# Optimization experiments

Hardware: AMD Instinct MI355X
Metric: run time of the kernel (lower is better)

The kernel has to match this reference:

```python
import jax, jax.numpy as jnp
import numpy as np

N_NODES = 50000
N_EDGES = 1600000
N_GRAPHS = 512
IN_DIM = 64
HID = 128
OUT_DIM = 10


def setup_inputs() -> dict:
    key = jax.random.key(0)
    ks = jax.random.split(key, 12)
    x = jax.random.normal(ks[0], (N_NODES, IN_DIM), dtype=jnp.float32)
    edge_index = jax.random.randint(ks[1], (2, N_EDGES), 0, N_NODES, dtype=jnp.int64)
    batch = jnp.sort(jax.random.randint(ks[2], (N_NODES,), 0, N_GRAPHS, dtype=jnp.int64))
    edge_attr = jax.random.uniform(ks[3], (N_EDGES,), dtype=jnp.float32)
    # glorot-ish init for weights
    def lin(k, fan_in, fan_out):
        s = (6.0 / (fan_in + fan_out)) ** 0.5
        return jax.random.uniform(k, (fan_in, fan_out), minval=-s, maxval=s, dtype=jnp.float32)
    return {
        "x": x, "edge_index": edge_index, "batch": batch, "edge_attr": edge_attr,
        "W1": lin(ks[4], IN_DIM, HID), "b1": jnp.zeros((HID,), jnp.float32),
        "W2": lin(ks[5], HID, HID), "b2": jnp.zeros((HID,), jnp.float32),
        "Wm1": lin(ks[6], HID, HID), "bm1": jnp.zeros((HID,), jnp.float32),
        "Wm2": lin(ks[7], HID, OUT_DIM), "bm2": jnp.zeros((OUT_DIM,), jnp.float32),
    }


def _gcn_conv(x, edge_index, edge_weight, W, b, num_nodes):
    """PyG GCNConv: add self-loops, symmetric norm with edge weights, x@W, scatter-add, +bias."""
    loop = jnp.arange(num_nodes, dtype=edge_index.dtype)
    src = jnp.concatenate([edge_index[0], loop])
    dst = jnp.concatenate([edge_index[1], loop])
    ew = jnp.concatenate([edge_weight, jnp.ones((num_nodes,), edge_weight.dtype)])
    deg = jax.ops.segment_sum(ew, dst, num_segments=num_nodes)  # [N]
    dinv = jnp.where(deg > 0, jax.lax.rsqrt(jnp.where(deg > 0, deg, 1.0)), 0.0)
    norm = dinv[src] * ew * dinv[dst]  # [E+N]
    h = x @ W  # [N, F_out]
    msg = h[src] * norm[:, None]  # gather + scale
    out = jax.ops.segment_sum(msg, dst, num_segments=num_nodes)
    return out + b


def reference(x, edge_index, batch, edge_attr, W1, b1, W2, b2, Wm1, bm1, Wm2, bm2):
    n = x.shape[0]
    h = _gcn_conv(x, edge_index, edge_attr, W1, b1, n)
    h = jax.nn.relu(h)  # dropout = identity in eval mode
    h = _gcn_conv(h, edge_index, edge_attr, W2, b2, n)
    h = jax.nn.relu(h)
    pooled = jax.ops.segment_sum(h, batch, num_segments=N_GRAPHS)  # global_add_pool
    z = jax.nn.relu(pooled @ Wm1 + bm1)
    return z @ Wm2 + bm2  # [num_graphs, out_dim]
```

## Files before the change

### kernel.cpp

```cpp
#include <hip/hip_runtime.h>
#include <hip/hip_bf16.h>
#include <hip/hip_fp16.h>
#include <cstdint>

#define HIDC 128
#define FIXSCALE 4194304.0f
#define FIXINV   (1.0f / 4194304.0f)
#define MAXDEG 80

#define BKT_SHIFT 7
#define BKT_NODES 128
#define BKT_CAP   6144
#define BIN_TILE  8192
#define BIN_THREADS 512

typedef _Float16 half8 __attribute__((ext_vector_type(8)));
typedef float float4v __attribute__((ext_vector_type(4)));

__global__ __launch_bounds__(BIN_THREADS) void bin_kernel(
        const int* __restrict__ ei, const float* __restrict__ ea,
        unsigned long long* __restrict__ buck, unsigned int* __restrict__ tails,
        int E, int nbkt) {
    __shared__ unsigned long long rec[BIN_TILE];
    __shared__ unsigned int cnt[BIN_THREADS];
    __shared__ unsigned int startx[BIN_THREADS];
    __shared__ unsigned int cur[BIN_THREADS];
    __shared__ unsigned int gbase[BIN_THREADS];
    int t = threadIdx.x;
    int base = blockIdx.x * BIN_TILE;
    int total = E - base; if (total > BIN_TILE) total = BIN_TILE;

    cnt[t] = 0;
    __syncthreads();

    unsigned int lo[16], dv[16];
#pragma unroll
    for (int j = 0; j < 16; ++j) {
        int e = base + j * BIN_THREADS + t;
        if (e < E) {
            int s = ei[e]; int d = ei[E + e]; float w = ea[e];
            lo[j] = (unsigned int)s |
                    ((unsigned int)__half_as_ushort(__float2half_rn(w)) << 16);
            dv[j] = (unsigned int)d;
            atomicAdd(&cnt[dv[j] >> BKT_SHIFT], 1u);
        } else dv[j] = 0xffffffffu;
    }
    __syncthreads();

    startx[t] = cnt[t];
    __syncthreads();
    for (int off = 1; off < BIN_THREADS; off <<= 1) {
        unsigned int add = (t >= off) ? startx[t - off] : 0u;
        __syncthreads();
        startx[t] += add;
        __syncthreads();
    }
    unsigned int excl = startx[t] - cnt[t];
    startx[t] = excl;
    cur[t] = excl;
    if (t < nbkt) gbase[t] = atomicAdd(&tails[t], cnt[t]);
    __syncthreads();

#pragma unroll
    for (int j = 0; j < 16; ++j) {
        if (dv[j] != 0xffffffffu) {
            unsigned int p = atomicAdd(&cur[dv[j] >> BKT_SHIFT], 1u);
            rec[p] = ((unsigned long long)dv[j] << 32) | (unsigned long long)lo[j];
        }
    }
    __syncthreads();

    for (int i = t; i < total; i += BIN_THREADS) {
        unsigned long long r = rec[i];
        unsigned int b = ((unsigned int)(r >> 32)) >> BKT_SHIFT;
        unsigned int idx = gbase[b] + ((unsigned int)i - startx[b]);
        if (idx < BKT_CAP) buck[(size_t)b * BKT_CAP + idx] = r;
    }
}

__global__ __launch_bounds__(256) void fill_kernel(
        const unsigned long long* __restrict__ buck,
        const unsigned int* __restrict__ tails,
        unsigned long long* __restrict__ degcnt,
        unsigned int* __restrict__ padcsr, int n_nodes) {
    __shared__ unsigned long long deg[BKT_NODES];
    int b = blockIdx.x, t = threadIdx.x;
    if (t < BKT_NODES) deg[t] = 0ull;
    __syncthreads();
    int cnt_b = (int)tails[b]; if (cnt_b > BKT_CAP) cnt_b = BKT_CAP;
    const unsigned long long* rb = buck + (size_t)b * BKT_CAP;
    int nodeBase = b << BKT_SHIFT;
    for (int i = t; i < cnt_b; i += 256) {
        unsigned long long r = rb[i];
        unsigned int lo = (unsigned int)r;
        unsigned int dl = ((unsigned int)(r >> 32)) & (BKT_NODES - 1);
        float w = __half2float(__ushort_as_half((unsigned short)(lo >> 16)));
        unsigned int fx = (unsigned int)(w * FIXSCALE + 0.5f);
        unsigned long long old =
            atomicAdd(&deg[dl], (1ull << 32) | (unsigned long long)fx);
        unsigned int rank = (unsigned int)(old >> 32);
        if (rank < MAXDEG)
            padcsr[(size_t)(nodeBase + dl) * MAXDEG + rank] = lo;
    }
    __syncthreads();
    if (t < BKT_NODES) {
        int node = nodeBase + t;
        if (node < n_nodes) degcnt[node] = deg[t];
    }
}

__global__ void transpose_w2_kernel(const float* __restrict__ W2,
                                    _Float16* __restrict__ W2t) {
    int i = blockIdx.x * 256 + threadIdx.x;
    int k = i >> 7, n = i & 127;
    W2t[n * 128 + k] = (_Float16)W2[i];
}

template <int K>
__global__ __launch_bounds__(256) void gemm_tiled(const float* __restrict__ A,
                                                  const float* __restrict__ W,
                                                  const unsigned long long* __restrict__ degcnt,
                                                  __half* __restrict__ out, int n_nodes) {
    __shared__ float sW[K * 128];
    __shared__ float sX[16 * K];
    int t = threadIdx.x;
    int nodeBase = blockIdx.x * 16;
    for (int i = t; i < K * 128; i += 256) sW[i] = W[i];
    int nAvail = n_nodes - nodeBase; if (nAvail > 16) nAvail = 16;
    for (int i = t; i < nAvail * K; i += 256) sX[i] = A[(size_t)nodeBase * K + i];
    __syncthreads();
    int d = t & 127;
    for (int ni = (t >> 7); ni < nAvail; ni += 2) {
        int node = nodeBase + ni;
        float acc = 0.f;
#pragma unroll
        for (int k = 0; k < K; ++k) acc += sX[ni * K + k] * sW[k * 128 + d];
        unsigned long long v = degcnt[node];
        float di = rsqrtf(1.0f + (float)(unsigned int)(v & 0xffffffffull) * FIXINV);
        out[(size_t)node * 128 + d] = __float2half(acc * di);
    }
}

__global__ __launch_bounds__(256) void gemm2_mfma_kernel(
        const __half* __restrict__ A,
        const _Float16* __restrict__ W2t,
        const unsigned long long* __restrict__ degcnt,
        __half* __restrict__ out, int n_nodes) {
    int wave = threadIdx.x >> 6, lane = threadIdx.x & 63;
    int nodeBase = (blockIdx.x * 4 + wave) * 16;
    if (nodeBase >= n_nodes) return;
    int mrow = lane & 15, quad = lane >> 4;

    int anode = nodeBase + mrow; if (anode >= n_nodes) anode = n_nodes - 1;
    const _Float16* Arow = (const _Float16*)A + (size_t)anode * 128 + quad * 8;
    half8 a[4];
#pragma unroll
    for (int q = 0; q < 4; ++q) a[q] = *(const half8*)(Arow + q * 32);

    float4v acc[8];
#pragma unroll
    for (int nt = 0; nt < 8; ++nt) acc[nt] = (float4v)(0.f);
#pragma unroll
    for (int nt = 0; nt < 8; ++nt) {
        const _Float16* Brow = W2t + (size_t)(nt * 16 + mrow) * 128 + quad * 8;
#pragma unroll
        for (int q = 0; q < 4; ++q) {
            half8 b = *(const half8*)(Brow + q * 32);
            acc[nt] = __builtin_amdgcn_mfma_f32_16x16x32_f16(a[q], b, acc[nt], 0, 0, 0);
        }
    }
#pragma unroll
    for (int r = 0; r < 4; ++r) {
        int node = nodeBase + quad * 4 + r;
        if (node < n_nodes) {
            unsigned long long v = degcnt[node];
            float di = rsqrtf(1.0f + (float)(unsigned int)(v & 0xffffffffull) * FIXINV);
#pragma unroll
            for (int nt = 0; nt < 8; ++nt)
                out[(size_t)node * 128 + nt * 16 + mrow] = __float2half(acc[nt][r] * di);
        }
    }
}

__global__ __launch_bounds__(256) void agg_kernel(const __half* __restrict__ h,
                                                  const unsigned long long* __restrict__ degcnt,
                                                  const unsigned int* __restrict__ padcsr,
                                                  const float* __restrict__ bias,
                                                  __half* __restrict__ out, int n_nodes) {
    int wave = threadIdx.x >> 6;
    int lane = threadIdx.x & 63;
    int node = blockIdx.x * 4 + wave;
    if (node >= n_nodes) return;
    unsigned long long v = degcnt[node];
    int cnt = (int)(v >> 32);
    float di = rsqrtf(1.0f + (float)(unsigned int)(v & 0xffffffffull) * FIXINV);
    const unsigned int* row = padcsr + (size_t)node * MAXDEG;
    float a0 = 0.f, a1 = 0.f;
    int e = 0;
    for (; e + 16 <= cnt; e += 16) {
        unsigned int p[16];
#pragma unroll
        for (int j = 0; j < 16; ++j) p[j] = row[e + j];
        __half2 vv[16];
#pragma unroll
        for (int j = 0; j < 16; ++j)
            vv[j] = *(reinterpret_cast<const __half2*>(h + (size_t)(p[j] & 0xffffu) * HIDC) + lane);
#pragma unroll
        for (int j = 0; j < 16; ++j) {
            float c = __half2float(__ushort_as_half((unsigned short)(p[j] >> 16)));
            float2 f = __half22float2(vv[j]);
            a0 += c * f.x; a1 += c * f.y;
        }
    }
    for (; e + 4 <= cnt; e += 4) {
        unsigned int p[4];
#pragma unroll
        for (int j = 0; j < 4; ++j) p[j] = row[e + j];
        __half2 vv[4];
#pragma unroll
        for (int j = 0; j < 4; ++j)
            vv[j] = *(reinterpret_cast<const __half2*>(h + (size_t)(p[j] & 0xffffu) * HIDC) + lane);
#pragma unroll
        for (int j = 0; j < 4; ++j) {
            float c = __half2float(__ushort_as_half((unsigned short)(p[j] >> 16)));
            float2 f = __half22float2(vv[j]);
            a0 += c * f.x; a1 += c * f.y;
        }
    }
    for (; e < cnt; ++e) {
        unsigned int p = row[e];
        float c = __half2float(__ushort_as_half((unsigned short)(p >> 16)));
        float2 f = __half22float2(*(reinterpret_cast<const __half2*>(h + (size_t)(p & 0xffffu) * HIDC) + lane));
        a0 += c * f.x; a1 += c * f.y;
    }
    float2 fn = __half22float2(*(reinterpret_cast<const __half2*>(h + (size_t)node * HIDC) + lane));
    a0 = di * (a0 + fn.x);
    a1 = di * (a1 + fn.y);
    float2 bb = *(reinterpret_cast<const float2*>(bias) + lane);
    a0 = fmaxf(a0 + bb.x, 0.f);
    a1 = fmaxf(a1 + bb.y, 0.f);
    *(reinterpret_cast<__half2*>(out + (size_t)node * HIDC) + lane) =
        __floats2half2_rn(a0, a1);
}

__global__ __launch_bounds__(128) void pool_mlp_kernel(const __half* __restrict__ h,
                                                       const int* __restrict__ batch,
                                                       const float* __restrict__ Wm1,
                                                       const float* __restrict__ bm1,
                                                       const float* __restrict__ Wm2,
                                                       const float* __restrict__ bm2,
                                                       float* __restrict__ out,
                                                       int n_nodes, int out_dim) {
    int g = blockIdx.x;
    int t = threadIdx.x;
    __shared__ int sb[2];
    if (t < 2) {
        int target = g + t;
        int lo = 0, hi = n_nodes;
        while (lo < hi) { int mid = (lo + hi) >> 1; if (batch[mid] < target) lo = mid + 1; else hi = mid; }
        sb[t] = lo;
    }
    __syncthreads();
    int beg = sb[0], end = sb[1];
    float p = 0.f;
    for (int i = beg; i < end; ++i) p += __half2float(h[(size_t)i * 128 + t]);
    __shared__ float row[128];
    __shared__ float z[128];
    row[t] = p;
    __syncthreads();
    float acc = bm1[t];
#pragma unroll 8
    for (int k = 0; k < 128; ++k) acc += row[k] * Wm1[k * 128 + t];
    z[t] = fmaxf(acc, 0.f);
    __syncthreads();
    if (t < out_dim) {
        float o = bm2[t];
#pragma unroll 8
        for (int k = 0; k < 128; ++k) o += z[k] * Wm2[k * out_dim + t];
        out[g * out_dim + t] = o;
    }
}

extern "C" void kernel_launch(void* const* d_in, const int* in_sizes, int n_in,
                              void* d_out, int out_size, void* d_ws, size_t ws_size,
                              hipStream_t stream) {
    const float* x   = (const float*)d_in[0];
    const int*   ei  = (const int*)d_in[1];
    const int*   bat = (const int*)d_in[2];
    const float* ea  = (const float*)d_in[3];
    const float* W1  = (const float*)d_in[4];
    const float* b1  = (const float*)d_in[5];
    const float* W2  = (const float*)d_in[6];
    const float* b2  = (const float*)d_in[7];
    const float* Wm1 = (const float*)d_in[8];
    const float* bm1 = (const float*)d_in[9];
    const float* Wm2 = (const float*)d_in[10];
    const float* bm2 = (const float*)d_in[11];
    float* out = (float*)d_out;

    const int N = in_sizes[2];
    const int E = in_sizes[1] / 2;
    const int N_GRAPHS = 512;
    const int OUT_DIM = out_size / N_GRAPHS;

    char* ws = (char*)d_ws;
    size_t off = 0;
    auto alloc = [&](size_t bytes) { char* p = ws + off; off += (bytes + 255) & ~size_t(255); return p; };
    __half* bufA    = (__half*)alloc((size_t)N * HIDC * 2);
    __half* bufR    = (__half*)alloc((size_t)N * HIDC * 2);
    unsigned int* padcsr = (unsigned int*)alloc((size_t)N * MAXDEG * 4);
    unsigned long long* degcnt = (unsigned long long*)alloc((size_t)N * 8);
    _Float16* W2t   = (_Float16*)alloc(128 * 128 * 2);
    unsigned int* tails = (unsigned int*)alloc(BIN_THREADS * 4);

    unsigned long long* buck = (unsigned long long*)bufA;
    int nbkt = (N + BKT_NODES - 1) >> BKT_SHIFT;

    hipMemsetAsync(tails, 0, (size_t)nbkt * 4, stream);
    int binBlocks = (E + BIN_TILE - 1) / BIN_TILE;
    bin_kernel<<<binBlocks, BIN_THREADS, 0, stream>>>(ei, ea, buck, tails, E, nbkt);
    fill_kernel<<<nbkt, 256, 0, stream>>>(buck, tails, degcnt, padcsr, N);
    transpose_w2_kernel<<<64, 256, 0, stream>>>(W2, W2t);
    gemm_tiled<64><<<(N + 15) / 16, 256, 0, stream>>>(x, W1, degcnt, bufA, N);
    agg_kernel<<<(N + 3) / 4, 256, 0, stream>>>(bufA, degcnt, padcsr, b1, bufR, N);
    gemm2_mfma_kernel<<<(N + 63) / 64, 256, 0, stream>>>(bufR, W2t, degcnt, bufA, N);
    agg_kernel<<<(N + 3) / 4, 256, 0, stream>>>(bufA, degcnt, padcsr, b2, bufR, N);
    pool_mlp_kernel<<<N_GRAPHS, 128, 0, stream>>>(bufR, bat, Wm1, bm1, Wm2, bm2, out, N, OUT_DIM);
}
```

Before: 309.6 us.

## Store hidden features in 32-wide column chunks and aggregate per chunk

Hidden feature buffers move from node-major [N,128] to four chunk-major [4][N,32] planes. The GEMM, MFMA, aggregation and pooling kernels all index the new layout. The aggregation now runs one 16-lane group per node per chunk, so each chunk's gather working set (about 3.2 MB) is more likely to stay in cache. The cost is four passes over the CSR and 64-byte gathers instead of 256-byte ones. The bin kernel tile is also halved to launch more blocks.

```diff
diff --git a/kernel.cpp b/kernel.cpp
--- a/kernel.cpp
+++ b/kernel.cpp
@@ -8,10 +8,13 @@
 #define FIXINV   (1.0f / 4194304.0f)
 #define MAXDEG 80
 
+#define NCHUNK 4
+#define CDIM 32
+
 #define BKT_SHIFT 7
 #define BKT_NODES 128
 #define BKT_CAP   6144
-#define BIN_TILE  8192
+#define BIN_TILE  4096
 #define BIN_THREADS 512
 
 typedef _Float16 half8 __attribute__((ext_vector_type(8)));
@@ -33,9 +36,9 @@
     cnt[t] = 0;
     __syncthreads();
 
-    unsigned int lo[16], dv[16];
-#pragma unroll
-    for (int j = 0; j < 16; ++j) {
+    unsigned int lo[8], dv[8];
+#pragma unroll
+    for (int j = 0; j < 8; ++j) {
         int e = base + j * BIN_THREADS + t;
         if (e < E) {
             int s = ei[e]; int d = ei[E + e]; float w = ea[e];
@@ -62,7 +65,7 @@
     __syncthreads();
 
 #pragma unroll
-    for (int j = 0; j < 16; ++j) {
+    for (int j = 0; j < 8; ++j) {
         if (dv[j] != 0xffffffffu) {
             unsigned int p = atomicAdd(&cur[dv[j] >> BKT_SHIFT], 1u);
             rec[p] = ((unsigned long long)dv[j] << 32) | (unsigned long long)lo[j];
@@ -130,6 +133,7 @@
     for (int i = t; i < nAvail * K; i += 256) sX[i] = A[(size_t)nodeBase * K + i];
     __syncthreads();
     int d = t & 127;
+    size_t cstride = (size_t)n_nodes * CDIM;
     for (int ni = (t >> 7); ni < nAvail; ni += 2) {
         int node = nodeBase + ni;
         float acc = 0.f;
@@ -137,7 +141,8 @@
         for (int k = 0; k < K; ++k) acc += sX[ni * K + k] * sW[k * 128 + d];
         unsigned long long v = degcnt[node];
         float di = rsqrtf(1.0f + (float)(unsigned int)(v & 0xffffffffull) * FIXINV);
-        out[(size_t)node * 128 + d] = __float2half(acc * di);
+        out[(size_t)(d >> 5) * cstride + (size_t)node * CDIM + (d & 31)] =
+            __float2half(acc * di);
     }
 }
 
@@ -150,12 +155,13 @@
     int nodeBase = (blockIdx.x * 4 + wave) * 16;
     if (nodeBase >= n_nodes) return;
     int mrow = lane & 15, quad = lane >> 4;
+    size_t cstride = (size_t)n_nodes * CDIM;
 
     int anode = nodeBase + mrow; if (anode >= n_nodes) anode = n_nodes - 1;
-    const _Float16* Arow = (const _Float16*)A + (size_t)anode * 128 + quad * 8;
+    const _Float16* Abase = (const _Float16*)A + (size_t)anode * CDIM + quad * 8;
     half8 a[4];
 #pragma unroll
-    for (int q = 0; q < 4; ++q) a[q] = *(const half8*)(Arow + q * 32);
+    for (int q = 0; q < 4; ++q) a[q] = *(const half8*)(Abase + q * cstride);
 
     float4v acc[8];
 #pragma unroll
@@ -177,70 +183,65 @@
             float di = rsqrtf(1.0f + (float)(unsigned int)(v & 0xffffffffull) * FIXINV);
 #pragma unroll
             for (int nt = 0; nt < 8; ++nt)
-                out[(size_t)node * 128 + nt * 16 + mrow] = __float2half(acc[nt][r] * di);
+                out[(size_t)(nt >> 1) * cstride + (size_t)node * CDIM +
+                    (nt & 1) * 16 + mrow] = __float2half(acc[nt][r] * di);
         }
     }
 }
 
-__global__ __launch_bounds__(256) void agg_kernel(const __half* __restrict__ h,
-                                                  const unsigned long long* __restrict__ degcnt,
-                                                  const unsigned int* __restrict__ padcsr,
-                                                  const float* __restrict__ bias,
-                                                  __half* __restrict__ out, int n_nodes) {
-    int wave = threadIdx.x >> 6;
-    int lane = threadIdx.x & 63;
-    int node = blockIdx.x * 4 + wave;
-    if (node >= n_nodes) return;
-    unsigned long long v = degcnt[node];
-    int cnt = (int)(v >> 32);
+__global__ __launch_bounds__(256) void agg_chunk_kernel(
+        const __half* __restrict__ h,
+        const unsigned long long* __restrict__ degcnt,
+        const unsigned int* __restrict__ padcsr,
+        const float* __restrict__ bias,
+        __half* __restrict__ out, int n_nodes, int ngroups) {
+    int chunk = blockIdx.x / ngroups;
+    int grp   = blockIdx.x - chunk * ngroups;
+    int t = threadIdx.x;
+    int lane16 = t & 15;
+    int node = grp * 16 + (t >> 4);
+    bool valid = node < n_nodes;
+    int nodeC = valid ? node : 0;
+    unsigned long long v = degcnt[nodeC];
+    int cnt = valid ? (int)(v >> 32) : 0;
+    if (cnt > MAXDEG) cnt = MAXDEG;
     float di = rsqrtf(1.0f + (float)(unsigned int)(v & 0xffffffffull) * FIXINV);
-    const unsigned int* row = padcsr + (size_t)node * MAXDEG;
+    const unsigned int* row = padcsr + (size_t)nodeC * MAXDEG;
+    const __half2* hc = (const __half2*)(h + (size_t)chunk * (size_t)n_nodes * CDIM);
+
     float a0 = 0.f, a1 = 0.f;
     int e = 0;
-    for (; e + 16 <= cnt; e += 16) {
-        unsigned int p[16];
-#pragma unroll
-        for (int j = 0; j < 16; ++j) p[j] = row[e + j];
-        __half2 vv[16];
-#pragma unroll
-        for (int j = 0; j < 16; ++j)
-            vv[j] = *(reinterpret_cast<const __half2*>(h + (size_t)(p[j] & 0xffffu) * HIDC) + lane);
-#pragma unroll
-        for (int j = 0; j < 16; ++j) {
+    for (; e + 8 <= cnt; e += 8) {
+        unsigned int p[8];
+#pragma unroll
+        for (int j = 0; j < 8; ++j) p[j] = row[e + j];
+        __half2 vv[8];
+#pragma unroll
+        for (int j = 0; j < 8; ++j)
+            vv[j] = hc[(p[j] & 0xffffu) * 16u + (unsigned)lane16];
+#pragma unroll
+        for (int j = 0; j < 8; ++j) {
             float c = __half2float(__ushort_as_half((unsigned short)(p[j] >> 16)));
             float2 f = __half22float2(vv[j]);
-            a0 += c * f.x; a1 += c * f.y;
-        }
-    }
-    for (; e + 4 <= cnt; e += 4) {
-        unsigned int p[4];
-#pragma unroll
-        for (int j = 0; j < 4; ++j) p[j] = row[e + j];
-        __half2 vv[4];
-#pragma unroll
-        for (int j = 0; j < 4; ++j)
-            vv[j] = *(reinterpret_cast<const __half2*>(h + (size_t)(p[j] & 0xffffu) * HIDC) + lane);
-#pragma unroll
-        for (int j = 0; j < 4; ++j) {
-            float c = __half2float(__ushort_as_half((unsigned short)(p[j] >> 16)));
-            float2 f = __half22float2(vv[j]);
-            a0 += c * f.x; a1 += c * f.y;
+            a0 = fmaf(c, f.x, a0); a1 = fmaf(c, f.y, a1);
         }
     }
     for (; e < cnt; ++e) {
         unsigned int p = row[e];
         float c = __half2float(__ushort_as_half((unsigned short)(p >> 16)));
-        float2 f = __half22float2(*(reinterpret_cast<const __half2*>(h + (size_t)(p & 0xffffu) * HIDC) + lane));
-        a0 += c * f.x; a1 += c * f.y;
-    }
-    float2 fn = __half22float2(*(reinterpret_cast<const __half2*>(h + (size_t)node * HIDC) + lane));
-    a0 = di * (a0 + fn.x);
-    a1 = di * (a1 + fn.y);
-    float2 bb = *(reinterpret_cast<const float2*>(bias) + lane);
-    a0 = fmaxf(a0 + bb.x, 0.f);
-    a1 = fmaxf(a1 + bb.y, 0.f);
-    *(reinterpret_cast<__half2*>(out + (size_t)node * HIDC) + lane) =
-        __floats2half2_rn(a0, a1);
+        float2 f = __half22float2(hc[(p & 0xffffu) * 16u + (unsigned)lane16]);
+        a0 = fmaf(c, f.x, a0); a1 = fmaf(c, f.y, a1);
+    }
+    if (valid) {
+        float2 fn = __half22float2(hc[(unsigned)node * 16u + (unsigned)lane16]);
+        a0 = di * (a0 + fn.x);
+        a1 = di * (a1 + fn.y);
+        float2 bb = *(reinterpret_cast<const float2*>(bias + chunk * CDIM) + lane16);
+        a0 = fmaxf(a0 + bb.x, 0.f);
+        a1 = fmaxf(a1 + bb.y, 0.f);
+        *((__half2*)(out + (size_t)chunk * (size_t)n_nodes * CDIM) +
+          (unsigned)node * 16u + lane16) = __floats2half2_rn(a0, a1);
+    }
 }
 
 __global__ __launch_bounds__(128) void pool_mlp_kernel(const __half* __restrict__ h,
@@ -262,8 +263,9 @@
     }
     __syncthreads();
     int beg = sb[0], end = sb[1];
+    const __half* hchunk = h + (size_t)(t >> 5) * (size_t)n_nodes * CDIM + (t & 31);
     float p = 0.f;
-    for (int i = beg; i < end; ++i) p += __half2float(h[(size_t)i * 128 + t]);
+    for (int i = beg; i < end; ++i) p += __half2float(hchunk[(size_t)i * CDIM]);
     __shared__ float row[128];
     __shared__ float z[128];
     row[t] = p;
@@ -322,8 +324,9 @@
     fill_kernel<<<nbkt, 256, 0, stream>>>(buck, tails, degcnt, padcsr, N);
     transpose_w2_kernel<<<64, 256, 0, stream>>>(W2, W2t);
     gemm_tiled<64><<<(N + 15) / 16, 256, 0, stream>>>(x, W1, degcnt, bufA, N);
-    agg_kernel<<<(N + 3) / 4, 256, 0, stream>>>(bufA, degcnt, padcsr, b1, bufR, N);
+    int ngroups = (N + 15) / 16;
+    agg_chunk_kernel<<<NCHUNK * ngroups, 256, 0, stream>>>(bufA, degcnt, padcsr, b1, bufR, N, ngroups);
     gemm2_mfma_kernel<<<(N + 63) / 64, 256, 0, stream>>>(bufR, W2t, degcnt, bufA, N);
-    agg_kernel<<<(N + 3) / 4, 256, 0, stream>>>(bufA, degcnt, padcsr, b2, bufR, N);
+    agg_chunk_kernel<<<NCHUNK * ngroups, 256, 0, stream>>>(bufA, degcnt, padcsr, b2, bufR, N, ngroups);
     pool_mlp_kernel<<<N_GRAPHS, 128, 0, stream>>>(bufR, bat, Wm1, bm1, Wm2, bm2, out, N, OUT_DIM);
 }
```

After: 322.5 us. 1.04x slower.
